# Kernel tuning notes

Measured on AMD Instinct MI355X. Metric: run time of the kernel, lower is better.

Reference implementation:

```python
import jax, jax.numpy as jnp
import numpy as np

POOL = 7              # pool_size -> output resolution
H, W, C = 200, 304, 256   # stride-16 feature map of a ~3200x4864 image
N = 2000              # number of RoIs


def setup_inputs() -> dict:
    key = jax.random.key(0)
    k1, k2, k3 = jax.random.split(key, 3)
    fmap = jax.random.normal(k1, (1, H, W, C), dtype=jnp.float32)
    # rois are (x0, y0, x1, y1) in IMAGE pixel coords; forward divides by stride.
    stride = 16
    xy0 = jax.random.uniform(k2, (N, 2), dtype=jnp.float32) * jnp.array([W * stride * 0.6, H * stride * 0.6], jnp.float32)
    wh = jax.random.uniform(k3, (N, 2), dtype=jnp.float32, minval=0.05, maxval=0.4) * jnp.array([W * stride * 0.4, H * stride * 0.4], jnp.float32)
    rois = jnp.concatenate([xy0, xy0 + wh], axis=1)
    return {"shared_layers": fmap, "rois": rois, "extractor_stride": 16}


def _roi_align(fmap, boxes, resolution):
    """fmap: [1,H,W,C]; boxes: [N,4] (x0,y0,x1,y1) fp-coords on the feature map.
    Replicates crop_and_resize(pad_border=True) at 2x resolution + 2x2 avg pool,
    then NCHW transpose + flatten, exactly as the TF module."""
    img = jnp.pad(fmap[0], ((1, 1), (1, 1), (0, 0)), mode="symmetric")  # [H+2, W+2, C]
    boxes = jax.lax.stop_gradient(boxes) + 1.0  # account for 1-pixel symmetric pad
    Hp, Wp, Cc = img.shape
    n = boxes.shape[0]
    S = resolution * 2
    x0, y0, x1, y1 = boxes[:, 0], boxes[:, 1], boxes[:, 2], boxes[:, 3]
    sw = (x1 - x0) / S
    sh = (y1 - y0) / S
    i = jnp.arange(S, dtype=jnp.float32)
    # fpcoor sample centers: x0 + spacing/2 - 0.5 + i*spacing (== TF transform_fpcoor_for_tf grid)
    ys = y0[:, None] + sh[:, None] * (i + 0.5) - 0.5  # [N,S]
    xs = x0[:, None] + sw[:, None] * (i + 0.5) - 0.5  # [N,S]

    def idx(coords, size):
        f0 = jnp.floor(coords)
        frac = coords - f0
        i0 = jnp.clip(f0.astype(jnp.int32), 0, size - 1)
        i1 = jnp.clip(i0 + 1, 0, size - 1)
        valid = (coords >= 0) & (coords <= size - 1)  # TF extrapolation_value = 0
        return i0, i1, frac, valid

    yi0, yi1, ly, vy = idx(ys, Hp)
    xi0, xi1, lx, vx = idx(xs, Wp)

    g = lambda yi, xi: img[yi[:, :, None], xi[:, None, :]]  # gather -> [N,S,S,C]
    ly_, lx_ = ly[:, :, None, None], lx[:, None, :, None]
    crop = ((1.0 - ly_) * ((1.0 - lx_) * g(yi0, xi0) + lx_ * g(yi0, xi1))
            + ly_ * ((1.0 - lx_) * g(yi1, xi0) + lx_ * g(yi1, xi1)))
    crop = crop * (vy[:, :, None] & vx[:, None, :])[..., None].astype(crop.dtype)
    # 2x2 avg pool over spatial dims -> [N,res,res,C]
    pooled = crop.reshape(n, resolution, 2, resolution, 2, Cc).mean(axis=(2, 4))
    # transpose([0,3,1,2]) to NCHW then Flatten -> [N, C*res*res]
    return pooled.transpose(0, 3, 1, 2).reshape(n, -1)


def reference(shared_layers, rois, extractor_stride):
    boxes = rois / jnp.float32(extractor_stride)  # feature-map fp-coords
    return _roi_align(shared_layers, boxes, POOL)
```

## Files before the change

kernel.cpp:

```cpp
#include <hip/hip_runtime.h>


#define HH 200
#define WW 304
#define CC 256
#define HP (HH + 2)
#define WP (WW + 2)
#define PS 14
#define NCELL 49
#define PROWS 25
#define PSTRIDE 289
#define NBUCKET 256

__global__ __launch_bounds__(256) void roi_sort_kernel(
    const float* __restrict__ rois,
    const int*   __restrict__ stride_p,
    int n, int* __restrict__ perm)
{
    __shared__ int hist[NBUCKET];
    __shared__ int scan[NBUCKET];
    __shared__ int offs[NBUCKET];
    const int t = threadIdx.x;
    hist[t] = 0;
    __syncthreads();

    const float inv = 1.0f / (float)stride_p[0];
    auto key_of = [&](int i) -> int {
        const float cx = 0.5f * (rois[4 * i + 0] + rois[4 * i + 2]) * inv;
        const float cy = 0.5f * (rois[4 * i + 1] + rois[4 * i + 3]) * inv;
        int tx = (int)(cx * (16.0f / (float)WW));
        int ty = (int)(cy * (16.0f / (float)HH));
        tx = min(max(tx, 0), 15);
        ty = min(max(ty, 0), 15);
        int k = 0;
#pragma unroll
        for (int b = 0; b < 4; ++b)
            k |= (((tx >> b) & 1) << (2 * b)) | (((ty >> b) & 1) << (2 * b + 1));
        return k;
    };

    for (int i = t; i < n; i += 256) atomicAdd(&hist[key_of(i)], 1);
    __syncthreads();

    scan[t] = hist[t];
    __syncthreads();
    for (int d = 1; d < NBUCKET; d <<= 1) {
        const int x = (t >= d) ? scan[t - d] : 0;
        __syncthreads();
        scan[t] += x;
        __syncthreads();
    }
    offs[t] = scan[t] - hist[t];
    __syncthreads();

    for (int i = t; i < n; i += 256) {
        const int pos = atomicAdd(&offs[key_of(i)], 1);
        perm[pos] = i;
    }
}

__global__ __launch_bounds__(256, 4) void roi_align_kernel(
    const float* __restrict__ fmap,
    const float* __restrict__ rois,
    const int*   __restrict__ stride_p,
    const int*   __restrict__ perm,
    int nwg,
    float*       __restrict__ out)
{
    __shared__ float pool[PROWS * PSTRIDE];
    __shared__ float wtab[NCELL * 16];
    __shared__ int   otab[NCELL * 16];
    __shared__ int   yo0[PS], yo1[PS], xo0[PS], xo1[PS];
    __shared__ float lyv[PS], vyv[PS], lxv[PS], vxv[PS];

    const int t = threadIdx.x;

    const int bid = blockIdx.x;
    const int q8 = nwg >> 3, rem = nwg & 7;
    const int xcd = bid & 7, idx8 = bid >> 3;
    const int swz = (xcd < rem ? xcd * (q8 + 1) : rem * (q8 + 1) + (xcd - rem) * q8) + idx8;
    const int r = perm[swz];

    if (t < 2 * PS) {
        const bool isx = (t >= PS);
        const int  i   = isx ? (t - PS) : t;
        const float inv = 1.0f / (float)stride_p[0];
        const float a0 = rois[4 * r + (isx ? 0 : 1)] * inv + 1.0f;
        const float a1 = rois[4 * r + (isx ? 2 : 3)] * inv + 1.0f;
        const float sc = (a1 - a0) / (float)PS;
        const float coord = a0 + sc * ((float)i + 0.5f) - 0.5f;
        const int size = isx ? WP : HP;

        const float f0   = floorf(coord);
        const float frac = coord - f0;
        int i0 = (int)f0;
        i0 = min(max(i0, 0), size - 1);
        const int i1 = min(i0 + 1, size - 1);
        const float valid = (coord >= 0.0f && coord <= (float)(size - 1)) ? 1.0f : 0.0f;

        if (isx) {
            xo0[i] = min(max(i0 - 1, 0), WW - 1) * CC;
            xo1[i] = min(max(i1 - 1, 0), WW - 1) * CC;
            lxv[i] = frac;
            vxv[i] = valid;
        } else {
            yo0[i] = min(max(i0 - 1, 0), HH - 1) * (WW * CC);
            yo1[i] = min(max(i1 - 1, 0), HH - 1) * (WW * CC);
            lyv[i] = frac;
            vyv[i] = valid;
        }
    }
    __syncthreads();

    if (t < NCELL * 4) {
        const int s  = t >> 2;
        const int qq = t & 3;
        const int dy = qq >> 1, dx = qq & 1;
        const int py = s / 7, px = s - py * 7;
        const int iy = 2 * py + dy, ix = 2 * px + dx;

        const float ly = lyv[iy], vy = vyv[iy];
        const float lx = lxv[ix], vx = vxv[ix];
        const float m = 0.25f * vy * vx;

        float4 w;
        w.x = m * (1.f - ly) * (1.f - lx);
        w.y = m * (1.f - ly) * lx;
        w.z = m * ly * (1.f - lx);
        w.w = m * ly * lx;
        int4 o;
        o.x = (yo0[iy] + xo0[ix]) >> 2;
        o.y = (yo0[iy] + xo1[ix]) >> 2;
        o.z = (yo1[iy] + xo0[ix]) >> 2;
        o.w = (yo1[iy] + xo1[ix]) >> 2;

        reinterpret_cast<float4*>(wtab)[t] = w;
        reinterpret_cast<int4*>(otab)[t]   = o;
    }
    __syncthreads();

    const int cg = t & 63;
    const int sq = t >> 6;
    const float4* __restrict__ f4 = reinterpret_cast<const float4*>(fmap);
    const float4* wt4 = reinterpret_cast<const float4*>(wtab);
    const int4*   ot4 = reinterpret_cast<const int4*>(otab);
    const size_t base = (size_t)r * (CC * NCELL);

#pragma unroll 1
    for (int phase = 0; phase < 2; ++phase) {
        const int s_lo = phase ? PROWS : 0;
        const int s_hi = phase ? NCELL : PROWS;
        const int nrow = s_hi - s_lo;

        for (int ss = s_lo + sq; ss < s_hi; ss += 8) {
            const int  s0   = ss;
            const bool has1 = (ss + 4) < s_hi;
            const int  s1   = has1 ? ss + 4 : ss;
            float4 acc0 = make_float4(0.f, 0.f, 0.f, 0.f);
            float4 acc1 = make_float4(0.f, 0.f, 0.f, 0.f);
#pragma unroll
            for (int qq = 0; qq < 4; ++qq) {
                const float4 w0 = wt4[s0 * 4 + qq];
                const int4   o0 = ot4[s0 * 4 + qq];
                const float4 w1 = wt4[s1 * 4 + qq];
                const int4   o1 = ot4[s1 * 4 + qq];

                const float4 a0 = f4[o0.x + cg];
                const float4 a1 = f4[o0.y + cg];
                const float4 a2 = f4[o0.z + cg];
                const float4 a3 = f4[o0.w + cg];
                const float4 b0 = f4[o1.x + cg];
                const float4 b1 = f4[o1.y + cg];
                const float4 b2 = f4[o1.z + cg];
                const float4 b3 = f4[o1.w + cg];

                acc0.x += w0.x * a0.x + w0.y * a1.x + w0.z * a2.x + w0.w * a3.x;
                acc0.y += w0.x * a0.y + w0.y * a1.y + w0.z * a2.y + w0.w * a3.y;
                acc0.z += w0.x * a0.z + w0.y * a1.z + w0.z * a2.z + w0.w * a3.z;
                acc0.w += w0.x * a0.w + w0.y * a1.w + w0.z * a2.w + w0.w * a3.w;
                acc1.x += w1.x * b0.x + w1.y * b1.x + w1.z * b2.x + w1.w * b3.x;
                acc1.y += w1.x * b0.y + w1.y * b1.y + w1.z * b2.y + w1.w * b3.y;
                acc1.z += w1.x * b0.z + w1.y * b1.z + w1.z * b2.z + w1.w * b3.z;
                acc1.w += w1.x * b0.w + w1.y * b1.w + w1.z * b2.w + w1.w * b3.w;
            }
            {
                const int row = s0 - s_lo;
                const int c0  = 4 * cg;
                const int col = c0 + (c0 >> 5);
                float* d0 = &pool[row * PSTRIDE + col];
                d0[0] = acc0.x; d0[1] = acc0.y; d0[2] = acc0.z; d0[3] = acc0.w;
            }
            if (has1) {
                const int row = s1 - s_lo;
                const int c0  = 4 * cg;
                const int col = c0 + (c0 >> 5);
                float* d1 = &pool[row * PSTRIDE + col];
                d1[0] = acc1.x; d1[1] = acc1.y; d1[2] = acc1.z; d1[3] = acc1.w;
            }
        }
        __syncthreads();

        const int total = nrow * CC;
#pragma unroll 1
        for (int e = t; e < total; e += 256) {
            const int c  = e / nrow;
            const int sp = e - c * nrow;
            out[base + c * NCELL + s_lo + sp] = pool[sp * PSTRIDE + c + (c >> 5)];
        }
        __syncthreads();
    }
}

extern "C" void kernel_launch(void* const* d_in, const int* in_sizes, int n_in,
                              void* d_out, int out_size, void* d_ws, size_t ws_size,
                              hipStream_t stream) {
    const float* fmap = (const float*)d_in[0];
    const float* rois = (const float*)d_in[1];
    const int*   strd = (const int*)d_in[2];
    float*       out  = (float*)d_out;
    int*         perm = (int*)d_ws;
    const int n = in_sizes[1] / 4;

    roi_sort_kernel<<<1, 256, 0, stream>>>(rois, strd, n, perm);
    roi_align_kernel<<<n, 256, 0, stream>>>(fmap, rois, strd, perm, n, out);
}
```

Before: 227.8 us.

## Split RoIAlign staging by channel halves with XOR-swizzled float4 LDS stores

```diff
diff --git a/kernel.cpp b/kernel.cpp
--- a/kernel.cpp
+++ b/kernel.cpp
@@ -8,8 +8,7 @@
 #define WP (WW + 2)
 #define PS 14
 #define NCELL 49
-#define PROWS 25
-#define PSTRIDE 289
+#define HALFC 128
 #define NBUCKET 256
 
 __global__ __launch_bounds__(256) void roi_sort_kernel(
@@ -59,7 +58,7 @@
     }
 }
 
-__global__ __launch_bounds__(256, 4) void roi_align_kernel(
+__global__ __launch_bounds__(256, 5) void roi_align_kernel(
     const float* __restrict__ fmap,
     const float* __restrict__ rois,
     const int*   __restrict__ stride_p,
@@ -67,9 +66,9 @@
     int nwg,
     float*       __restrict__ out)
 {
-    __shared__ float pool[PROWS * PSTRIDE];
-    __shared__ float wtab[NCELL * 16];
-    __shared__ int   otab[NCELL * 16];
+    __shared__ alignas(16) float pool[NCELL * HALFC];
+    __shared__ alignas(16) float wtab[NCELL * 16];
+    __shared__ alignas(16) int   otab[NCELL * 16];
     __shared__ int   yo0[PS], yo1[PS], xo0[PS], xo1[PS];
     __shared__ float lyv[PS], vyv[PS], lxv[PS], vxv[PS];
 
@@ -139,40 +138,38 @@
     }
     __syncthreads();
 
-    const int cg = t & 63;
-    const int sq = t >> 6;
+    const int slot = t >> 5;
+    const int cg2  = t & 31;
     const float4* __restrict__ f4 = reinterpret_cast<const float4*>(fmap);
     const float4* wt4 = reinterpret_cast<const float4*>(wtab);
     const int4*   ot4 = reinterpret_cast<const int4*>(otab);
+    float4* pool4 = reinterpret_cast<float4*>(pool);
     const size_t base = (size_t)r * (CC * NCELL);
 
 #pragma unroll 1
-    for (int phase = 0; phase < 2; ++phase) {
-        const int s_lo = phase ? PROWS : 0;
-        const int s_hi = phase ? NCELL : PROWS;
-        const int nrow = s_hi - s_lo;
-
-        for (int ss = s_lo + sq; ss < s_hi; ss += 8) {
-            const int  s0   = ss;
-            const bool has1 = (ss + 4) < s_hi;
-            const int  s1   = has1 ? ss + 4 : ss;
+    for (int ph = 0; ph < 2; ++ph) {
+        const int phbase = ph * 32 + cg2;
+
+        for (int s = slot; s < NCELL; s += 16) {
+            const bool has1 = (s + 8) < NCELL;
+            const int  s1   = has1 ? s + 8 : s;
             float4 acc0 = make_float4(0.f, 0.f, 0.f, 0.f);
             float4 acc1 = make_float4(0.f, 0.f, 0.f, 0.f);
 #pragma unroll
             for (int qq = 0; qq < 4; ++qq) {
-                const float4 w0 = wt4[s0 * 4 + qq];
-                const int4   o0 = ot4[s0 * 4 + qq];
+                const float4 w0 = wt4[s * 4 + qq];
+                const int4   o0 = ot4[s * 4 + qq];
                 const float4 w1 = wt4[s1 * 4 + qq];
                 const int4   o1 = ot4[s1 * 4 + qq];
 
-                const float4 a0 = f4[o0.x + cg];
-                const float4 a1 = f4[o0.y + cg];
-                const float4 a2 = f4[o0.z + cg];
-                const float4 a3 = f4[o0.w + cg];
-                const float4 b0 = f4[o1.x + cg];
-                const float4 b1 = f4[o1.y + cg];
-                const float4 b2 = f4[o1.z + cg];
-                const float4 b3 = f4[o1.w + cg];
+                const float4 a0 = f4[o0.x + phbase];
+                const float4 a1 = f4[o0.y + phbase];
+                const float4 a2 = f4[o0.z + phbase];
+                const float4 a3 = f4[o0.w + phbase];
+                const float4 b0 = f4[o1.x + phbase];
+                const float4 b1 = f4[o1.y + phbase];
+                const float4 b2 = f4[o1.z + phbase];
+                const float4 b3 = f4[o1.w + phbase];
 
                 acc0.x += w0.x * a0.x + w0.y * a1.x + w0.z * a2.x + w0.w * a3.x;
                 acc0.y += w0.x * a0.y + w0.y * a1.y + w0.z * a2.y + w0.w * a3.y;
@@ -183,29 +180,19 @@
                 acc1.z += w1.x * b0.z + w1.y * b1.z + w1.z * b2.z + w1.w * b3.z;
                 acc1.w += w1.x * b0.w + w1.y * b1.w + w1.z * b2.w + w1.w * b3.w;
             }
-            {
-                const int row = s0 - s_lo;
-                const int c0  = 4 * cg;
-                const int col = c0 + (c0 >> 5);
-                float* d0 = &pool[row * PSTRIDE + col];
-                d0[0] = acc0.x; d0[1] = acc0.y; d0[2] = acc0.z; d0[3] = acc0.w;
-            }
-            if (has1) {
-                const int row = s1 - s_lo;
-                const int c0  = 4 * cg;
-                const int col = c0 + (c0 >> 5);
-                float* d1 = &pool[row * PSTRIDE + col];
-                d1[0] = acc1.x; d1[1] = acc1.y; d1[2] = acc1.z; d1[3] = acc1.w;
-            }
+            pool4[s * 32 + (cg2 ^ (s & 7))] = acc0;
+            if (has1)
+                pool4[s1 * 32 + (cg2 ^ (s1 & 7))] = acc1;
         }
         __syncthreads();
 
-        const int total = nrow * CC;
 #pragma unroll 1
-        for (int e = t; e < total; e += 256) {
-            const int c  = e / nrow;
-            const int sp = e - c * nrow;
-            out[base + c * NCELL + s_lo + sp] = pool[sp * PSTRIDE + c + (c >> 5)];
+        for (int e = t; e < NCELL * HALFC; e += 256) {
+            const int c_loc = e / NCELL;
+            const int sp    = e - c_loc * NCELL;
+            const int u     = (c_loc >> 2) ^ (sp & 7);
+            const float v   = pool[sp * HALFC + (u << 2) + (c_loc & 3)];
+            out[base + (size_t)(ph * HALFC + c_loc) * NCELL + sp] = v;
         }
         __syncthreads();
     }
```

New measurement: 215.6 us. -5.3%, faster.
